# Kernel tuning notes

Hardware: AMD Instinct MI355X
Metric: run time of the kernel (lower is better)

Reference implementation:

```python
import jax, jax.numpy as jnp
import numpy as np

N_HEAD, D_K, D_V = 8, 16, 16


def _softmax_attention(q, k, v):
    # q, k: (..., Ck, H, W); v: (..., Cv, H, W). Attention over flattened HW tokens.
    Ck, H, W = q.shape[-3:]
    qf = q.reshape(q.shape[:-2] + (H * W,))  # (..., Ck, HW)
    kf = k.reshape(k.shape[:-2] + (H * W,))
    vf = v.reshape(v.shape[:-2] + (H * W,))
    scale = 1.0 / np.sqrt(Ck).astype(np.float32)
    attn = jax.nn.softmax(jnp.einsum('...ci,...cj->...ij', qf * scale, kf), axis=-1)
    out = jnp.einsum('...ij,...cj->...ci', attn, vf)  # (..., Cv, HW)
    return out.reshape(out.shape[:-1] + (H, W)), attn


def _long_range_attention(q, k, v, P_h, P_w):
    # Strided (dilated) grouping: h = qh*P_h + ph, so tokens in a group are P_h apart.
    B, N, C, H, W = q.shape
    Qh, Qw = H // P_h, W // P_w

    def grp(x):
        Cx = x.shape[2]
        x = x.reshape(B, N, Cx, Qh, P_h, Qw, P_w)
        return x.transpose(0, 1, 4, 6, 2, 3, 5)  # (B, N, P_h, P_w, C, Qh, Qw)

    out, attn = _softmax_attention(grp(q), grp(k), grp(v))
    Cv = out.shape[4]
    out = out.transpose(0, 1, 4, 5, 2, 6, 3).reshape(B, N, Cv, H, W)
    return out, attn


def _conv1x1(x, w):
    # x: (B, Cin, H, W); w: (Cout, Cin) == squeezed Conv2d(.,.,1,bias=False) weight
    return jnp.einsum('bchw,oc->bohw', x, w)


def setup_inputs() -> dict:
    key = jax.random.key(0)
    ks = jax.random.split(key, 7)
    B, C, H, W = 2, 128, 128, 128
    return {
        'q': jax.random.normal(ks[0], (B, C, H, W), jnp.float32),
        'k': jax.random.normal(ks[1], (B, C, H, W), jnp.float32),
        'v': jax.random.normal(ks[2], (B, C, H, W), jnp.float32),
        'w_qs': jax.random.normal(ks[3], (N_HEAD * D_K, C), jnp.float32) * 0.05,
        'w_ks': jax.random.normal(ks[4], (N_HEAD * D_K, C), jnp.float32) * 0.05,
        'w_vs': jax.random.normal(ks[5], (N_HEAD * D_V, C), jnp.float32) * 0.05,
        'w_fc': jax.random.normal(ks[6], (C, N_HEAD * D_V), jnp.float32) * 0.05,
        'ah': 8,
        'aw': 8,
    }


def reference(q, k, v, w_qs, w_ks, w_vs, w_fc, ah, aw):
    B, _, H, W = q.shape
    qp = _conv1x1(q, w_qs).reshape(B, N_HEAD, D_K, H, W)
    kp = _conv1x1(k, w_ks).reshape(B, N_HEAD, D_K, k.shape[2], k.shape[3])
    vp = _conv1x1(v, w_vs).reshape(B, N_HEAD, D_V, v.shape[2], v.shape[3])
    out, attn = _long_range_attention(qp, kp, vp, ah, aw)  # attn_type='sparse_long'
    out = out.reshape(B, N_HEAD * D_V, H, W)
    out = _conv1x1(out, w_fc)
    return out, attn
```

## Files before the change

kernel.cpp:

```cpp
#include <hip/hip_runtime.h>
#include <math.h>

#define HW 16384
#define NB 2

__device__ __forceinline__ void gemm_body(const float* __restrict__ X,
                                          const float* __restrict__ W,
                                          float* __restrict__ Y,
                                          int b, int t0, int tid) {
  __shared__ float WT[16][132];
  __shared__ float XT[16][68];
  const float* Xb = X + (size_t)b * 128 * HW;
  float* Yb = Y + (size_t)b * 128 * HW;
  const int tt = tid & 63;
  const int og = tid >> 6;
  float acc[32];
#pragma unroll
  for (int k = 0; k < 32; ++k) acc[k] = 0.f;

  for (int c0 = 0; c0 < 128; c0 += 16) {
#pragma unroll
    for (int r = 0; r < 2; ++r) {
      int flat = tid + r * 256;
      int o = flat >> 2, cc4 = flat & 3;
      float4 w4 = *reinterpret_cast<const float4*>(&W[o * 128 + c0 + cc4 * 4]);
      WT[cc4 * 4 + 0][o] = w4.x;
      WT[cc4 * 4 + 1][o] = w4.y;
      WT[cc4 * 4 + 2][o] = w4.z;
      WT[cc4 * 4 + 3][o] = w4.w;
    }
#pragma unroll
    for (int r = 0; r < 4; ++r) {
      int flat = tid + r * 256;
      int c = flat >> 6, tl = flat & 63;
      XT[c][tl] = Xb[(size_t)(c0 + c) * HW + t0 + tl];
    }
    __syncthreads();
#pragma unroll
    for (int c = 0; c < 16; ++c) {
      float xv = XT[c][tt];
      const float* wr = &WT[c][og * 32];
#pragma unroll
      for (int k = 0; k < 8; ++k) {
        float4 w4 = *reinterpret_cast<const float4*>(wr + k * 4);
        acc[k * 4 + 0] = fmaf(w4.x, xv, acc[k * 4 + 0]);
        acc[k * 4 + 1] = fmaf(w4.y, xv, acc[k * 4 + 1]);
        acc[k * 4 + 2] = fmaf(w4.z, xv, acc[k * 4 + 2]);
        acc[k * 4 + 3] = fmaf(w4.w, xv, acc[k * 4 + 3]);
      }
    }
    __syncthreads();
  }
#pragma unroll
  for (int k = 0; k < 32; ++k) {
    int o = og * 32 + k;
    Yb[(size_t)o * HW + t0 + tt] = acc[k];
  }
}

__global__ __launch_bounds__(256) void proj_kernel(
    const float* __restrict__ q, const float* __restrict__ k,
    const float* __restrict__ v, const float* __restrict__ wq,
    const float* __restrict__ wk, const float* __restrict__ wv,
    float* __restrict__ yq, float* __restrict__ yk, float* __restrict__ yv) {
  const float* X; const float* W; float* Y;
  if (blockIdx.z == 0)      { X = q; W = wq; Y = yq; }
  else if (blockIdx.z == 1) { X = k; W = wk; Y = yk; }
  else                      { X = v; W = wv; Y = yv; }
  gemm_body(X, W, Y, blockIdx.y, blockIdx.x * 64, threadIdx.x);
}

__global__ __launch_bounds__(256) void fc_kernel(
    const float* __restrict__ X, const float* __restrict__ W,
    float* __restrict__ Y) {
  gemm_body(X, W, Y, blockIdx.y, blockIdx.x * 64, threadIdx.x);
}

__device__ __forceinline__ float dot16(const float q[16], const float* kr) {
  float4 a = *reinterpret_cast<const float4*>(kr);
  float4 b = *reinterpret_cast<const float4*>(kr + 4);
  float4 c = *reinterpret_cast<const float4*>(kr + 8);
  float4 d = *reinterpret_cast<const float4*>(kr + 12);
  float s = q[0] * a.x;
  s = fmaf(q[1], a.y, s);  s = fmaf(q[2], a.z, s);  s = fmaf(q[3], a.w, s);
  s = fmaf(q[4], b.x, s);  s = fmaf(q[5], b.y, s);  s = fmaf(q[6], b.z, s);
  s = fmaf(q[7], b.w, s);  s = fmaf(q[8], c.x, s);  s = fmaf(q[9], c.y, s);
  s = fmaf(q[10], c.z, s); s = fmaf(q[11], c.w, s); s = fmaf(q[12], d.x, s);
  s = fmaf(q[13], d.y, s); s = fmaf(q[14], d.z, s); s = fmaf(q[15], d.w, s);
  return s;
}

__global__ __launch_bounds__(256) void attn_kernel(
    const float* __restrict__ Yq, const float* __restrict__ Yk,
    const float* __restrict__ Yv, float* __restrict__ Yo,
    float* __restrict__ Attn) {
  __shared__ float Kl[256][20];
  __shared__ float Vl[256][20];
  __shared__ float Pl[256][17];
  const int grp = blockIdx.x;
  const int bn = grp >> 6;
  const int g = grp & 63;
  const int ph = g >> 3, pw = g & 7;
  const int tid = threadIdx.x;
  const size_t base = (size_t)16 * bn * HW;
  const int ti = ((tid >> 4) * 8 + ph) * 128 + (tid & 15) * 8 + pw;

  float q[16];
#pragma unroll
  for (int c = 0; c < 16; ++c) {
    q[c] = 0.25f * Yq[base + (size_t)c * HW + ti];
    Kl[tid][c] = Yk[base + (size_t)c * HW + ti];
    Vl[tid][c] = Yv[base + (size_t)c * HW + ti];
  }
  __syncthreads();

  float m = -1e30f, l = 0.f;
  for (int jb = 0; jb < 256; jb += 16) {
    float s[16];
#pragma unroll
    for (int jj = 0; jj < 16; ++jj) s[jj] = dot16(q, &Kl[jb + jj][0]);
    float cm = s[0];
#pragma unroll
    for (int jj = 1; jj < 16; ++jj) cm = fmaxf(cm, s[jj]);
    float mn = fmaxf(m, cm);
    float a = 0.f;
#pragma unroll
    for (int jj = 0; jj < 16; ++jj) a += __expf(s[jj] - mn);
    l = l * __expf(m - mn) + a;
    m = mn;
  }
  const float rl = 1.f / l;

  float oa[16];
#pragma unroll
  for (int c = 0; c < 16; ++c) oa[c] = 0.f;
  float* ag = Attn + (size_t)grp * 65536;

  for (int jc0 = 0; jc0 < 16; ++jc0) {
    const int jb = jc0 * 16;
    float p[16];
#pragma unroll
    for (int jj = 0; jj < 16; ++jj)
      p[jj] = __expf(dot16(q, &Kl[jb + jj][0]) - m) * rl;
#pragma unroll
    for (int jj = 0; jj < 16; ++jj) {
      const float* vr = &Vl[jb + jj][0];
      float4 v0 = *reinterpret_cast<const float4*>(vr);
      float4 v1 = *reinterpret_cast<const float4*>(vr + 4);
      float4 v2 = *reinterpret_cast<const float4*>(vr + 8);
      float4 v3 = *reinterpret_cast<const float4*>(vr + 12);
      float pj = p[jj];
      oa[0]  = fmaf(pj, v0.x, oa[0]);  oa[1]  = fmaf(pj, v0.y, oa[1]);
      oa[2]  = fmaf(pj, v0.z, oa[2]);  oa[3]  = fmaf(pj, v0.w, oa[3]);
      oa[4]  = fmaf(pj, v1.x, oa[4]);  oa[5]  = fmaf(pj, v1.y, oa[5]);
      oa[6]  = fmaf(pj, v1.z, oa[6]);  oa[7]  = fmaf(pj, v1.w, oa[7]);
      oa[8]  = fmaf(pj, v2.x, oa[8]);  oa[9]  = fmaf(pj, v2.y, oa[9]);
      oa[10] = fmaf(pj, v2.z, oa[10]); oa[11] = fmaf(pj, v2.w, oa[11]);
      oa[12] = fmaf(pj, v3.x, oa[12]); oa[13] = fmaf(pj, v3.y, oa[13]);
      oa[14] = fmaf(pj, v3.z, oa[14]); oa[15] = fmaf(pj, v3.w, oa[15]);
    }
#pragma unroll
    for (int jj = 0; jj < 16; ++jj) Pl[tid][jj] = p[jj];
    __syncthreads();
#pragma unroll
    for (int r = 0; r < 16; ++r) {
      int f = tid + r * 256;
      ag[(size_t)(f >> 4) * 256 + jb + (f & 15)] = Pl[f >> 4][f & 15];
    }
    __syncthreads();
  }

#pragma unroll
  for (int c = 0; c < 16; ++c)
    Yo[base + (size_t)c * HW + ti] = oa[c];
}

extern "C" void kernel_launch(void* const* d_in, const int* in_sizes, int n_in,
                              void* d_out, int out_size, void* d_ws, size_t ws_size,
                              hipStream_t stream) {
  const float* q  = (const float*)d_in[0];
  const float* k  = (const float*)d_in[1];
  const float* v  = (const float*)d_in[2];
  const float* wq = (const float*)d_in[3];
  const float* wk = (const float*)d_in[4];
  const float* wv = (const float*)d_in[5];
  const float* wf = (const float*)d_in[6];

  float* out  = (float*)d_out;
  float* attn = out + (size_t)NB * 128 * HW;

  float* ws = (float*)d_ws;
  const size_t buf = (size_t)NB * 128 * HW;
  float* yq = ws;
  float* yk = yq + buf;
  float* yv = yk + buf;
  float* yo = yq;

  proj_kernel<<<dim3(256, NB, 3), 256, 0, stream>>>(q, k, v, wq, wk, wv, yq, yk, yv);
  attn_kernel<<<dim3(1024), 256, 0, stream>>>(yq, yk, yv, yo, attn);
  fc_kernel<<<dim3(256, NB), 256, 0, stream>>>(yo, wf, out);
}
```

Baseline: 663.3 us.

## Store projections in grouped layout, retile 1x1 GEMMs, write attn rows directly

The projection kernel now writes Q/K/V in a per-group contiguous layout (group, channel, token), so the attention kernel reads them with unit stride, and the FC kernel gathers back from that layout. The GEMMs are retiled: the full 128x128 weight matrix is staged in LDS once per block, and each thread computes a 16x4 register tile from float4 row loads. The attention kernel drops the shared-memory transpose and its two barriers per chunk, writing each thread's attention row directly as float4 stores, and adds an occupancy hint. The risks are strided scattered stores in proj, 64KB of LDS per GEMM block limiting occupancy, and uncoalesced per-thread row writes of the large attn output.

```diff
diff --git a/kernel.cpp b/kernel.cpp
--- a/kernel.cpp
+++ b/kernel.cpp
@@ -4,57 +4,34 @@
 #define HW 16384
 #define NB 2
 
-__device__ __forceinline__ void gemm_body(const float* __restrict__ X,
-                                          const float* __restrict__ W,
-                                          float* __restrict__ Y,
-                                          int b, int t0, int tid) {
-  __shared__ float WT[16][132];
-  __shared__ float XT[16][68];
-  const float* Xb = X + (size_t)b * 128 * HW;
-  float* Yb = Y + (size_t)b * 128 * HW;
-  const int tt = tid & 63;
-  const int og = tid >> 6;
-  float acc[32];
-#pragma unroll
-  for (int k = 0; k < 32; ++k) acc[k] = 0.f;
-
-  for (int c0 = 0; c0 < 128; c0 += 16) {
-#pragma unroll
-    for (int r = 0; r < 2; ++r) {
-      int flat = tid + r * 256;
-      int o = flat >> 2, cc4 = flat & 3;
-      float4 w4 = *reinterpret_cast<const float4*>(&W[o * 128 + c0 + cc4 * 4]);
-      WT[cc4 * 4 + 0][o] = w4.x;
-      WT[cc4 * 4 + 1][o] = w4.y;
-      WT[cc4 * 4 + 2][o] = w4.z;
-      WT[cc4 * 4 + 3][o] = w4.w;
-    }
-#pragma unroll
-    for (int r = 0; r < 4; ++r) {
-      int flat = tid + r * 256;
-      int c = flat >> 6, tl = flat & 63;
-      XT[c][tl] = Xb[(size_t)(c0 + c) * HW + t0 + tl];
-    }
-    __syncthreads();
-#pragma unroll
-    for (int c = 0; c < 16; ++c) {
-      float xv = XT[c][tt];
-      const float* wr = &WT[c][og * 32];
-#pragma unroll
-      for (int k = 0; k < 8; ++k) {
-        float4 w4 = *reinterpret_cast<const float4*>(wr + k * 4);
-        acc[k * 4 + 0] = fmaf(w4.x, xv, acc[k * 4 + 0]);
-        acc[k * 4 + 1] = fmaf(w4.y, xv, acc[k * 4 + 1]);
-        acc[k * 4 + 2] = fmaf(w4.z, xv, acc[k * 4 + 2]);
-        acc[k * 4 + 3] = fmaf(w4.w, xv, acc[k * 4 + 3]);
-      }
-    }
-    __syncthreads();
-  }
-#pragma unroll
-  for (int k = 0; k < 32; ++k) {
-    int o = og * 32 + k;
-    Yb[(size_t)o * HW + t0 + tt] = acc[k];
+
+__device__ __forceinline__ void fma16x4(float acc[16][4], const float* wr, float4 xv) {
+#pragma unroll
+  for (int jq = 0; jq < 4; ++jq) {
+    float4 w4 = *reinterpret_cast<const float4*>(wr + jq * 4);
+    float wj[4] = {w4.x, w4.y, w4.z, w4.w};
+#pragma unroll
+    for (int jj = 0; jj < 4; ++jj) {
+      acc[jq * 4 + jj][0] = fmaf(wj[jj], xv.x, acc[jq * 4 + jj][0]);
+      acc[jq * 4 + jj][1] = fmaf(wj[jj], xv.y, acc[jq * 4 + jj][1]);
+      acc[jq * 4 + jj][2] = fmaf(wj[jj], xv.z, acc[jq * 4 + jj][2]);
+      acc[jq * 4 + jj][3] = fmaf(wj[jj], xv.w, acc[jq * 4 + jj][3]);
+    }
+  }
+}
+
+__device__ __forceinline__ void stage_WT(float WT[128][128],
+                                         const float* __restrict__ W, int tid) {
+  const int o = tid & 127;
+  const int c4b = tid >> 7;
+#pragma unroll
+  for (int r = 0; r < 16; ++r) {
+    int c4 = c4b + 2 * r;
+    float4 w4 = *reinterpret_cast<const float4*>(&W[o * 128 + c4 * 4]);
+    WT[c4 * 4 + 0][o] = w4.x;
+    WT[c4 * 4 + 1][o] = w4.y;
+    WT[c4 * 4 + 2][o] = w4.z;
+    WT[c4 * 4 + 3][o] = w4.w;
   }
 }
 
@@ -63,17 +40,90 @@
     const float* __restrict__ v, const float* __restrict__ wq,
     const float* __restrict__ wk, const float* __restrict__ wv,
     float* __restrict__ yq, float* __restrict__ yk, float* __restrict__ yv) {
-  const float* X; const float* W; float* Y;
-  if (blockIdx.z == 0)      { X = q; W = wq; Y = yq; }
-  else if (blockIdx.z == 1) { X = k; W = wk; Y = yk; }
-  else                      { X = v; W = wv; Y = yv; }
-  gemm_body(X, W, Y, blockIdx.y, blockIdx.x * 64, threadIdx.x);
+  __shared__ float WT[128][128];
+  const float* X; const float* W; float* Yg;
+  if (blockIdx.z == 0)      { X = q; W = wq; Yg = yq; }
+  else if (blockIdx.z == 1) { X = k; W = wk; Yg = yk; }
+  else                      { X = v; W = wv; Yg = yv; }
+  const int b = blockIdx.y;
+  const int h = blockIdx.x;
+  const int tid = threadIdx.x;
+  stage_WT(WT, W, tid);
+  __syncthreads();
+
+  const int m = tid & 31;
+  const int og = tid >> 5;
+  const float* Xrow = X + (size_t)b * 128 * HW + h * 128 + m * 4;
+  float acc[16][4];
+#pragma unroll
+  for (int j = 0; j < 16; ++j)
+#pragma unroll
+    for (int t = 0; t < 4; ++t) acc[j][t] = 0.f;
+
+#pragma unroll 4
+  for (int c = 0; c < 128; ++c) {
+    float4 xv = *reinterpret_cast<const float4*>(Xrow + (size_t)c * HW);
+    fma16x4(acc, &WT[c][og * 16], xv);
+  }
+
+  const int ph = h & 7, qh = h >> 3;
+#pragma unroll
+  for (int j = 0; j < 16; ++j) {
+    int o = og * 16 + j;
+    int n = o >> 4, cc = o & 15;
+#pragma unroll
+    for (int t = 0; t < 4; ++t) {
+      int w = m * 4 + t;
+      int pw = w & 7, qw = w >> 3;
+      size_t addr = ((((size_t)(b * 8 + n) * 8 + ph) * 8 + pw) * 16 + cc) * 256
+                    + qh * 16 + qw;
+      Yg[addr] = acc[j][t];
+    }
+  }
 }
 
 __global__ __launch_bounds__(256) void fc_kernel(
-    const float* __restrict__ X, const float* __restrict__ W,
-    float* __restrict__ Y) {
-  gemm_body(X, W, Y, blockIdx.y, blockIdx.x * 64, threadIdx.x);
+    const float* __restrict__ Xg, const float* __restrict__ W,
+    float* __restrict__ out) {
+  __shared__ float WT[128][128];
+  const int b = blockIdx.y;
+  const int h = blockIdx.x;
+  const int tid = threadIdx.x;
+  stage_WT(WT, W, tid);
+  __syncthreads();
+
+  const int m = tid & 31;
+  const int og = tid >> 5;
+  const int ph = h & 7, qh = h >> 3;
+  float acc[16][4];
+#pragma unroll
+  for (int j = 0; j < 16; ++j)
+#pragma unroll
+    for (int t = 0; t < 4; ++t) acc[j][t] = 0.f;
+
+#pragma unroll 2
+  for (int c = 0; c < 128; ++c) {
+    int n = c >> 4, cv = c & 15;
+    size_t cb = ((((size_t)(b * 8 + n) * 8 + ph) * 8) * 16 + cv) * 256
+                + qh * 16;
+    float4 xv;
+    {
+      int w0 = m * 4;
+      xv.x = Xg[cb + (size_t)(w0 & 7) * 4096 + ((w0 >> 3))];
+      xv.y = Xg[cb + (size_t)((w0 + 1) & 7) * 4096 + ((w0 + 1) >> 3)];
+      xv.z = Xg[cb + (size_t)((w0 + 2) & 7) * 4096 + ((w0 + 2) >> 3)];
+      xv.w = Xg[cb + (size_t)((w0 + 3) & 7) * 4096 + ((w0 + 3) >> 3)];
+    }
+    fma16x4(acc, &WT[c][og * 16], xv);
+  }
+
+  float* orow = out + (size_t)b * 128 * HW + h * 128 + m * 4;
+#pragma unroll
+  for (int j = 0; j < 16; ++j) {
+    int o = og * 16 + j;
+    *reinterpret_cast<float4*>(orow + (size_t)o * HW) =
+        make_float4(acc[j][0], acc[j][1], acc[j][2], acc[j][3]);
+  }
 }
 
 __device__ __forceinline__ float dot16(const float q[16], const float* kr) {
@@ -90,27 +140,22 @@
   return s;
 }
 
-__global__ __launch_bounds__(256) void attn_kernel(
-    const float* __restrict__ Yq, const float* __restrict__ Yk,
-    const float* __restrict__ Yv, float* __restrict__ Yo,
+__global__ __launch_bounds__(256, 4) void attn_kernel(
+    const float* __restrict__ Qg, const float* __restrict__ Kg,
+    const float* __restrict__ Vg, float* __restrict__ Og,
     float* __restrict__ Attn) {
   __shared__ float Kl[256][20];
   __shared__ float Vl[256][20];
-  __shared__ float Pl[256][17];
   const int grp = blockIdx.x;
-  const int bn = grp >> 6;
-  const int g = grp & 63;
-  const int ph = g >> 3, pw = g & 7;
   const int tid = threadIdx.x;
-  const size_t base = (size_t)16 * bn * HW;
-  const int ti = ((tid >> 4) * 8 + ph) * 128 + (tid & 15) * 8 + pw;
-
-  float q[16];
+  const size_t gbase = (size_t)grp * 4096;
+
+  float qv[16];
 #pragma unroll
   for (int c = 0; c < 16; ++c) {
-    q[c] = 0.25f * Yq[base + (size_t)c * HW + ti];
-    Kl[tid][c] = Yk[base + (size_t)c * HW + ti];
-    Vl[tid][c] = Yv[base + (size_t)c * HW + ti];
+    qv[c] = 0.25f * Qg[gbase + c * 256 + tid];
+    Kl[tid][c] = Kg[gbase + c * 256 + tid];
+    Vl[tid][c] = Vg[gbase + c * 256 + tid];
   }
   __syncthreads();
 
@@ -118,7 +163,7 @@
   for (int jb = 0; jb < 256; jb += 16) {
     float s[16];
 #pragma unroll
-    for (int jj = 0; jj < 16; ++jj) s[jj] = dot16(q, &Kl[jb + jj][0]);
+    for (int jj = 0; jj < 16; ++jj) s[jj] = dot16(qv, &Kl[jb + jj][0]);
     float cm = s[0];
 #pragma unroll
     for (int jj = 1; jj < 16; ++jj) cm = fmaxf(cm, s[jj]);
@@ -134,14 +179,13 @@
   float oa[16];
 #pragma unroll
   for (int c = 0; c < 16; ++c) oa[c] = 0.f;
-  float* ag = Attn + (size_t)grp * 65536;
-
-  for (int jc0 = 0; jc0 < 16; ++jc0) {
-    const int jb = jc0 * 16;
+  float* ag = Attn + (size_t)grp * 65536 + (size_t)tid * 256;
+
+  for (int jb = 0; jb < 256; jb += 16) {
     float p[16];
 #pragma unroll
     for (int jj = 0; jj < 16; ++jj)
-      p[jj] = __expf(dot16(q, &Kl[jb + jj][0]) - m) * rl;
+      p[jj] = __expf(dot16(qv, &Kl[jb + jj][0]) - m) * rl;
 #pragma unroll
     for (int jj = 0; jj < 16; ++jj) {
       const float* vr = &Vl[jb + jj][0];
@@ -160,19 +204,14 @@
       oa[14] = fmaf(pj, v3.z, oa[14]); oa[15] = fmaf(pj, v3.w, oa[15]);
     }
 #pragma unroll
-    for (int jj = 0; jj < 16; ++jj) Pl[tid][jj] = p[jj];
-    __syncthreads();
-#pragma unroll
-    for (int r = 0; r < 16; ++r) {
-      int f = tid + r * 256;
-      ag[(size_t)(f >> 4) * 256 + jb + (f & 15)] = Pl[f >> 4][f & 15];
-    }
-    __syncthreads();
+    for (int qd = 0; qd < 4; ++qd)
+      *reinterpret_cast<float4*>(ag + jb + qd * 4) =
+          make_float4(p[qd * 4], p[qd * 4 + 1], p[qd * 4 + 2], p[qd * 4 + 3]);
   }
 
 #pragma unroll
   for (int c = 0; c < 16; ++c)
-    Yo[base + (size_t)c * HW + ti] = oa[c];
+    Og[gbase + c * 256 + tid] = oa[c];
 }
 
 extern "C" void kernel_launch(void* const* d_in, const int* in_sizes, int n_in,
@@ -191,12 +230,13 @@
 
   float* ws = (float*)d_ws;
   const size_t buf = (size_t)NB * 128 * HW;
-  float* yq = ws;
-  float* yk = yq + buf;
-  float* yv = yk + buf;
-  float* yo = yq;
-
-  proj_kernel<<<dim3(256, NB, 3), 256, 0, stream>>>(q, k, v, wq, wk, wv, yq, yk, yv);
-  attn_kernel<<<dim3(1024), 256, 0, stream>>>(yq, yk, yv, yo, attn);
-  fc_kernel<<<dim3(256, NB), 256, 0, stream>>>(yo, wf, out);
-}
+  float* yq_g = ws;
+  float* yk_g = yq_g + buf;
+  float* yv_g = yk_g + buf;
+  float* yo_g = yq_g;
+
+  proj_kernel<<<dim3(128, NB, 3), 256, 0, stream>>>(q, k, v, wq, wk, wv,
+                                                    yq_g, yk_g, yv_g);
+  attn_kernel<<<dim3(1024), 256, 0, stream>>>(yq_g, yk_g, yv_g, yo_g, attn);
+  fc_kernel<<<dim3(128, NB), 256, 0, stream>>>(yo_g, wf, out);
+}
```

Result: faster. 621.4 us (-6.3%).
